# Kernel optimization log

Hardware: AMD Instinct MI355X
Metric: run time of the kernel (lower is better)

The kernel has to match this reference:

```python
import jax, jax.numpy as jnp
import numpy as np

IN_F = 512
OUT_F = 512
ALPHA = 0.2  # LeakyReLU negative slope
# dropout p=0.1 is a no-op at inference (training=False), so omitted


def setup_inputs() -> dict:
    key = jax.random.key(0)
    k1, k2, k3 = jax.random.split(key, 3)
    B, N = 16, 1024
    x = jax.random.normal(k1, (B, N, IN_F), dtype=jnp.float32)
    # xavier_uniform with gain=1.414
    limW = 1.414 * np.sqrt(6.0 / (IN_F + OUT_F))
    W = jax.random.uniform(k2, (IN_F, OUT_F), minval=-limW, maxval=limW, dtype=jnp.float32)
    lima = 1.414 * np.sqrt(6.0 / (2 * OUT_F + 1))
    a = jax.random.uniform(k3, (2 * OUT_F, 1), minval=-lima, maxval=lima, dtype=jnp.float32)
    beta = jnp.ones((1,), dtype=jnp.float32)
    return {"x": x, "W": W, "a": a, "beta": beta}


def reference(x, W, a, beta):
    # h: [B, N, F]
    h = jnp.matmul(x, W)
    # Split attention vector: e_ij = leakyrelu(h_i . a1 + h_j . a2)
    a1 = a[:OUT_F, 0]   # [F]
    a2 = a[OUT_F:, 0]   # [F]
    s1 = jnp.einsum('bnf,f->bn', h, a1)  # [B, N]
    s2 = jnp.einsum('bnf,f->bn', h, a2)  # [B, N]
    e = s1[:, :, None] + s2[:, None, :]  # [B, N, N]
    e = jnp.where(e > 0, e, ALPHA * e)   # LeakyReLU
    attention = jax.nn.softmax(e, axis=2)
    h_prime = jnp.einsum('bnm,bmf->bnf', attention, h)
    out = jax.nn.elu(h_prime + beta * h)
    return out
```

## Files before the change

### kernel.cpp

```cpp
#include <hip/hip_runtime.h>

using u16 = unsigned short;
using u32 = unsigned int;
using u64 = unsigned long long;

#define ALPHA 0.2f
#define LOG2E 1.4426950408889634f

typedef __bf16 bf16x8 __attribute__((ext_vector_type(8)));
typedef float f32x4 __attribute__((ext_vector_type(4)));
typedef float f32x16 __attribute__((ext_vector_type(16)));

__device__ __forceinline__ u16 f2bf(float f) {
  u32 u = __builtin_bit_cast(u32, f);
  u += 0x7FFFu + ((u >> 16) & 1u);
  return (u16)(u >> 16);
}
__device__ __forceinline__ float bf2f(u16 h) {
  u32 u = ((u32)h) << 16;
  return __builtin_bit_cast(float, u);
}
__device__ __forceinline__ void gload_lds16(const void* g, void* l) {
  __builtin_amdgcn_global_load_lds((__attribute__((address_space(1))) void*)g,
                                   (__attribute__((address_space(3))) void*)l,
                                   16, 0, 0);
}

__global__ __launch_bounds__(256) void k_cast_wT(const float* __restrict__ W, u16* __restrict__ wbt) {
  int idx = blockIdx.x * 256 + threadIdx.x;
  int k = idx >> 9, n = idx & 511;
  wbt[n * 512 + k] = f2bf(W[idx]);
}

__global__ __launch_bounds__(256, 2) void k_gemm1(const float* __restrict__ x, const u16* __restrict__ wbt,
                                                  const float* __restrict__ a,
                                                  u16* __restrict__ hbf,
                                                  float* __restrict__ s1p, float* __restrict__ s2p) {
  __shared__ __attribute__((aligned(16))) char lds[73728];
  __shared__ __attribute__((aligned(16))) float a_l[256];

  const int t = threadIdx.x;
  const int lane = t & 63;
  const int w = t >> 6;
  const int l31 = lane & 31, lhi = lane >> 5;
  const int rb = w >> 1, cg = w & 1;
  const int g = blockIdx.x;
  const int cb = (g >> 3) & 3;
  const int tile_m = (g & 7) | ((g >> 5) << 3);
  const int row0 = tile_m * 128;
  const int col0 = cb * 128;

  a_l[t] = (t < 128) ? a[col0 + t] : a[512 + col0 + (t - 128)];

  f32x16 acc[2][2];
#pragma unroll
  for (int i = 0; i < 2; ++i)
#pragma unroll
    for (int j = 0; j < 2; ++j)
#pragma unroll
      for (int r = 0; r < 16; ++r) acc[i][j][r] = 0.f;

#define STAGE_G1(kt, Ab, Bb)                                                              \
  {                                                                                       \
    const int k0_ = (kt) * 32;                                                            \
    _Pragma("unroll")                                                                     \
    for (int i = 0; i < 4; ++i) {                                                         \
      int G = i * 256 + t;                                                                \
      int row = G >> 3, ks = G & 7;                                                       \
      gload_lds16(x + (size_t)(row0 + row) * 512 + k0_ + ((ks ^ (row & 7)) * 4),          \
                  (Ab) + (size_t)(i * 256 + w * 64) * 16);                                \
    }                                                                                     \
    _Pragma("unroll")                                                                     \
    for (int i = 0; i < 2; ++i) {                                                         \
      int G = i * 256 + t;                                                                \
      int col = G >> 2, ks = G & 3;                                                       \
      gload_lds16(wbt + (size_t)(col0 + col) * 512 + k0_ + ((ks ^ ((col >> 1) & 3)) * 8), \
                  (Bb) + (size_t)(i * 256 + w * 64) * 16);                                \
    }                                                                                     \
  }

#define COMPUTE_G1(Ab, Bb)                                                                         \
  {                                                                                                \
    _Pragma("unroll")                                                                              \
    for (int ks = 0; ks < 2; ++ks) {                                                               \
      bf16x8 af[2];                                                                                \
      _Pragma("unroll")                                                                            \
      for (int sub = 0; sub < 2; ++sub) {                                                          \
        const int arow = rb * 64 + sub * 32 + l31;                                                 \
        const int kg = ks * 4 + lhi * 2;                                                           \
        f32x4 fa0 = *reinterpret_cast<const f32x4*>((Ab) + (size_t)(arow * 8 + (kg ^ (arow & 7))) * 16); \
        f32x4 fa1 = *reinterpret_cast<const f32x4*>((Ab) + (size_t)(arow * 8 + ((kg + 1) ^ (arow & 7))) * 16); \
        _Pragma("unroll")                                                                          \
        for (int jj = 0; jj < 4; ++jj) {                                                           \
          af[sub][jj] = (__bf16)fa0[jj];                                                           \
          af[sub][jj + 4] = (__bf16)fa1[jj];                                                       \
        }                                                                                          \
      }                                                                                            \
      bf16x8 bfr[2];                                                                               \
      _Pragma("unroll")                                                                            \
      for (int bt = 0; bt < 2; ++bt) {                                                             \
        const int bcol = cg * 64 + bt * 32 + l31;                                                  \
        const int kslot = (ks * 2 + lhi) ^ ((bcol >> 1) & 3);                                      \
        bfr[bt] = *reinterpret_cast<const bf16x8*>((Bb) + (size_t)(bcol * 4 + kslot) * 16);        \
      }                                                                                            \
      _Pragma("unroll")                                                                            \
      for (int sub = 0; sub < 2; ++sub)                                                            \
        _Pragma("unroll")                                                                          \
        for (int bt = 0; bt < 2; ++bt)                                                             \
          acc[sub][bt] = __builtin_amdgcn_mfma_f32_32x32x16_bf16(af[sub], bfr[bt], acc[sub][bt], 0, 0, 0); \
    }                                                                                              \
  }

  char* Ac = lds;             char* Bc = lds + 49152;
  char* An = lds + 16384;     char* Bn = lds + 57344;
  char* As = lds + 32768;     char* Bs = lds + 65536;

  STAGE_G1(0, Ac, Bc);
  STAGE_G1(1, An, Bn);
  __builtin_amdgcn_sched_barrier(0);
  asm volatile("s_waitcnt vmcnt(6) lgkmcnt(0)" ::: "memory");
  __builtin_amdgcn_s_barrier();
  __builtin_amdgcn_sched_barrier(0);

#pragma unroll 1
  for (int kt = 0; kt < 14; ++kt) {
    STAGE_G1(kt + 2, As, Bs);
    COMPUTE_G1(Ac, Bc);
    __builtin_amdgcn_sched_barrier(0);
    asm volatile("s_waitcnt vmcnt(6)" ::: "memory");
    __builtin_amdgcn_s_barrier();
    __builtin_amdgcn_sched_barrier(0);
    char* ta = Ac; Ac = An; An = As; As = ta;
    char* tb = Bc; Bc = Bn; Bn = Bs; Bs = tb;
  }
  COMPUTE_G1(Ac, Bc);
  __builtin_amdgcn_sched_barrier(0);
  asm volatile("s_waitcnt vmcnt(0)" ::: "memory");
  __builtin_amdgcn_s_barrier();
  __builtin_amdgcn_sched_barrier(0);
  COMPUTE_G1(An, Bn);
#undef STAGE_G1
#undef COMPUTE_G1

  __syncthreads();

  u16* lT = (u16*)lds;
#pragma unroll
  for (int sub = 0; sub < 2; ++sub)
#pragma unroll
    for (int bt = 0; bt < 2; ++bt) {
      const int col = cg * 64 + bt * 32 + l31;
#pragma unroll
      for (int r = 0; r < 16; ++r) {
        int row = rb * 64 + sub * 32 + (r & 3) + 8 * (r >> 2) + 4 * lhi;
        lT[row * 136 + col] = f2bf(acc[sub][bt][r]);
      }
    }
  __syncthreads();

#pragma unroll
  for (int i = 0; i < 8; ++i) {
    int G = i * 256 + t;
    int row = G >> 4, gg = G & 15;
    uint4 v = *reinterpret_cast<const uint4*>(&lT[row * 136 + gg * 8]);
    *reinterpret_cast<uint4*>(&hbf[(size_t)(row0 + row) * 512 + col0 + gg * 8]) = v;
  }
  {
    const int r2 = t >> 1, half = t & 1;
    float d1 = 0.f, d2 = 0.f;
#pragma unroll
    for (int i = 0; i < 8; ++i) {
      uint4 v = *reinterpret_cast<const uint4*>(&lT[r2 * 136 + half * 64 + i * 8]);
      u32 wds[4] = {v.x, v.y, v.z, v.w};
#pragma unroll
      for (int jj = 0; jj < 8; ++jj) {
        float h = bf2f((u16)(wds[jj >> 1] >> ((jj & 1) * 16)));
        d1 += h * a_l[half * 64 + i * 8 + jj];
        d2 += h * a_l[128 + half * 64 + i * 8 + jj];
      }
    }
    d1 += __shfl_xor(d1, 1);
    d2 += __shfl_xor(d2, 1);
    if (half == 0) {
      s1p[cb * 16384 + row0 + r2] = d1;
      s2p[cb * 16384 + row0 + r2] = d2;
    }
  }
}

__global__ __launch_bounds__(1024) void k_prep(const float* __restrict__ s1p, const float* __restrict__ s2p,
                                               float* __restrict__ e1s, float* __restrict__ e2s,
                                               u32* __restrict__ permM, u32* __restrict__ kng,
                                               float* __restrict__ c1ig, float* __restrict__ c2ig) {
  __shared__ u32 sk[1024];
  __shared__ float s2all[1024];
  __shared__ float s2sv[1024];
  __shared__ float arrA[1024];
  __shared__ float arrB[1024];
  const int b = blockIdx.x;
  const int t = threadIdx.x;
  const int id = b * 1024 + t;

  const float s1v = (s1p[id] + s1p[16384 + id] + s1p[32768 + id] + s1p[49152 + id]) * LOG2E;
  const float s2v = (s2p[id] + s2p[16384 + id] + s2p[32768 + id] + s2p[49152 + id]) * LOG2E;
  s2all[t] = s2v;

  {
    u32 bits = __builtin_bit_cast(u32, s2v);
    u32 key = (bits & 0x80000000u) ? ~bits : (bits | 0x80000000u);
    sk[t] = (key & 0xFFFFFC00u) | (u32)t;
  }
  for (int size = 2; size <= 1024; size <<= 1)
    for (int stride = size >> 1; stride > 0; stride >>= 1) {
      __syncthreads();
      int ixj = t ^ stride;
      if (ixj > t) {
        u32 va = sk[t], vb = sk[ixj];
        bool asc = ((t & size) == 0);
        if ((va > vb) == asc) { sk[t] = vb; sk[ixj] = va; }
      }
    }
  __syncthreads();

  const u32 idx = sk[t] & 1023u;
  const float sv = s2all[idx];
  s2sv[t] = sv;
  __syncthreads();

  const float E1 = exp2f(sv), E2 = exp2f(ALPHA * sv);
  e1s[b * 1024 + t] = E1;
  e2s[b * 1024 + t] = E2;
  permM[b * 1024 + t] = idx;
  arrA[t] = E2;
  arrB[t] = exp2f(s2sv[1023 - t]);
  __syncthreads();

  for (int off = 1; off < 1024; off <<= 1) {
    float aA = (t >= off) ? arrA[t - off] : 0.f;
    float aB = (t >= off) ? arrB[t - off] : 0.f;
    __syncthreads();
    arrA[t] += aA;
    arrB[t] += aB;
    __syncthreads();
  }

  {
    const float thr = -s1v;
    int lo = 0, hi = 1024;
    while (lo < hi) { int mid = (lo + hi) >> 1; if (s2sv[mid] <= thr) lo = mid + 1; else hi = mid; }
    const int kn = lo;
    float se1suf = (kn == 1024) ? 0.f : arrB[1023 - kn];
    float se2pre = (kn == 0) ? 0.f : arrA[kn - 1];
    const float c1 = exp2f(s1v), c2 = exp2f(ALPHA * s1v);
    const float inv = 1.0f / (c1 * se1suf + c2 * se2pre);
    c1ig[id] = c1 * inv;
    c2ig[id] = c2 * inv;
    kng[id] = (u32)kn;
  }
}

__global__ __launch_bounds__(256, 2) void k_sweep2(const u16* __restrict__ hbf,
                                                   const float* __restrict__ e1s, const float* __restrict__ e2s,
                                                   const u32* __restrict__ permM, const u32* __restrict__ kng,
                                                   const float* __restrict__ c1ig, const float* __restrict__ c2ig,
                                                   const float* __restrict__ betag, float* __restrict__ out) {
  __shared__ u16 Cp1[1025][16];
  __shared__ u16 Cp2[1025][16];
  __shared__ float c1i_l[1024];
  __shared__ float c2i_l[1024];
  __shared__ u16 kn_l[1024];
  __shared__ float segS1[16][16];
  __shared__ float segP2[16][16];

  const int t = threadIdx.x;
  const int B = blockIdx.x;
  const int b = (B & 7) * 2 + ((B >> 3) & 1);
  const int fc = B >> 4;

  const u16* hB = hbf + (size_t)b * 1024 * 512 + fc * 16;

#pragma unroll
  for (int q = 0; q < 4; ++q) {
    int i = q * 256 + t;
    c1i_l[i] = c1ig[b * 1024 + i];
    c2i_l[i] = c2ig[b * 1024 + i];
    kn_l[i] = (u16)kng[b * 1024 + i];
  }

  const int f = t & 15;
  const int seg = t >> 4;
  const int i0 = seg * 64;
  const u32* permB = permM + b * 1024 + i0;
  const float* e1B = e1s + b * 1024 + i0;
  const float* e2B = e2s + b * 1024 + i0;

  u32 hpk[32];
  float ss1 = 0.f, ss2 = 0.f;
#pragma unroll 8
  for (int c = 0; c < 64; c += 2) {
    u16 h0 = hB[(size_t)permB[c] * 512 + f];
    u16 h1 = hB[(size_t)permB[c + 1] * 512 + f];
    hpk[c >> 1] = (u32)h0 | ((u32)h1 << 16);
    ss1 = fmaf(e1B[c], bf2f(h0), ss1);
    ss1 = fmaf(e1B[c + 1], bf2f(h1), ss1);
    ss2 = fmaf(e2B[c], bf2f(h0), ss2);
    ss2 = fmaf(e2B[c + 1], bf2f(h1), ss2);
  }
  segS1[seg][f] = ss1;
  segP2[seg][f] = ss2;
  __syncthreads();

  float sufAfter = 0.f, preBefore = 0.f;
#pragma unroll
  for (int s7 = 0; s7 < 16; ++s7) {
    if (s7 > seg) sufAfter += segS1[s7][f];
    if (s7 < seg) preBefore += segP2[s7][f];
  }

  if (seg == 15) Cp1[1024][f] = 0;
  {
    float run1 = sufAfter;
#pragma unroll
    for (int c = 63; c >= 0; --c) {
      u16 hv = (u16)((hpk[c >> 1] >> ((c & 1) * 16)) & 0xFFFFu);
      run1 = fmaf(e1B[c], bf2f(hv), run1);
      Cp1[i0 + c][f] = f2bf(run1);
    }
  }
  {
    float run2 = preBefore;
#pragma unroll
    for (int c = 0; c < 64; ++c) {
      Cp2[i0 + c][f] = f2bf(run2);
      u16 hv = (u16)((hpk[c >> 1] >> ((c & 1) * 16)) & 0xFFFFu);
      run2 = fmaf(e2B[c], bf2f(hv), run2);
    }
    if (seg == 15) Cp2[1024][f] = f2bf(run2);
  }
  __syncthreads();

  const float beta = betag[0];
  const int nl = t >> 4;
#pragma unroll 4
  for (int r = 0; r < 64; ++r) {
    const int n = r * 16 + nl;
    const int kn = kn_l[n];
    const float A = bf2f(Cp1[kn][f]);
    const float Bv = bf2f(Cp2[kn][f]);
    const float hvn = bf2f(hB[(size_t)n * 512 + f]);
    const float xv = c1i_l[n] * A + c2i_l[n] * Bv + beta * hvn;
    out[((size_t)b * 1024 + n) * 512 + fc * 16 + f] = xv > 0.f ? xv : __expf(xv) - 1.0f;
  }
}

extern "C" void kernel_launch(void* const* d_in, const int* in_sizes, int n_in,
                              void* d_out, int out_size, void* d_ws, size_t ws_size,
                              hipStream_t stream) {
  const float* x = (const float*)d_in[0];
  const float* W = (const float*)d_in[1];
  const float* a = (const float*)d_in[2];
  const float* beta = (const float*)d_in[3];
  float* out = (float*)d_out;

  char* ws = (char*)d_ws;
  u16* hbf = (u16*)ws;
  char* sm = ws + (16u << 20);
  float* e1s = (float*)(sm);
  float* e2s = (float*)(sm + (64u << 10));
  u32* permM = (u32*)(sm + (128u << 10));
  u32* kng = (u32*)(sm + (192u << 10));
  float* c1i = (float*)(sm + (256u << 10));
  float* c2i = (float*)(sm + (320u << 10));
  float* s1p = (float*)(sm + (512u << 10));
  float* s2p = (float*)(sm + (768u << 10));
  u16* wbt = (u16*)(sm + (1024u << 10));

  k_cast_wT<<<1024, 256, 0, stream>>>(W, wbt);
  k_gemm1<<<512, 256, 0, stream>>>(x, wbt, a, hbf, s1p, s2p);
  k_prep<<<16, 1024, 0, stream>>>(s1p, s2p, e1s, e2s, permM, kng, c1i, c2i);
  k_sweep2<<<512, 256, 0, stream>>>(hbf, e1s, e2s, permM, kng, c1i, c2i, beta, out);
}
```

Before: 66.64 us.

## Double sweep block size, interleave prefix arrays in padded LDS, read coefficients from global

The sweep kernel now runs 512 threads per block, so each thread scans a 32-row segment instead of 64. This shortens the serial prefix/suffix chains and halves per-thread register arrays. The two bf16 prefix arrays are packed into one padded u32 LDS array, so the final pass needs a single LDS read per row. The per-row coefficient and split-index staging in LDS is removed in favour of direct global loads. The trade-off is extra global traffic for those coefficients in the output loop, plus a longer cross-segment reduction over 32 segments.

```diff
diff --git a/kernel.cpp b/kernel.cpp
--- a/kernel.cpp
+++ b/kernel.cpp
@@ -259,18 +259,14 @@
   }
 }
 
-__global__ __launch_bounds__(256, 2) void k_sweep2(const u16* __restrict__ hbf,
+__global__ __launch_bounds__(512, 2) void k_sweep2(const u16* __restrict__ hbf,
                                                    const float* __restrict__ e1s, const float* __restrict__ e2s,
                                                    const u32* __restrict__ permM, const u32* __restrict__ kng,
                                                    const float* __restrict__ c1ig, const float* __restrict__ c2ig,
                                                    const float* __restrict__ betag, float* __restrict__ out) {
-  __shared__ u16 Cp1[1025][16];
-  __shared__ u16 Cp2[1025][16];
-  __shared__ float c1i_l[1024];
-  __shared__ float c2i_l[1024];
-  __shared__ u16 kn_l[1024];
-  __shared__ float segS1[16][16];
-  __shared__ float segP2[16][16];
+  __shared__ u32 Cp[1025][17];
+  __shared__ float segS1[32][16];
+  __shared__ float segP2[32][16];
 
   const int t = threadIdx.x;
   const int B = blockIdx.x;
@@ -279,25 +275,17 @@
 
   const u16* hB = hbf + (size_t)b * 1024 * 512 + fc * 16;
 
-#pragma unroll
-  for (int q = 0; q < 4; ++q) {
-    int i = q * 256 + t;
-    c1i_l[i] = c1ig[b * 1024 + i];
-    c2i_l[i] = c2ig[b * 1024 + i];
-    kn_l[i] = (u16)kng[b * 1024 + i];
-  }
-
   const int f = t & 15;
   const int seg = t >> 4;
-  const int i0 = seg * 64;
+  const int i0 = seg * 32;
   const u32* permB = permM + b * 1024 + i0;
   const float* e1B = e1s + b * 1024 + i0;
   const float* e2B = e2s + b * 1024 + i0;
 
-  u32 hpk[32];
+  u32 hpk[16];
   float ss1 = 0.f, ss2 = 0.f;
-#pragma unroll 8
-  for (int c = 0; c < 64; c += 2) {
+#pragma unroll
+  for (int c = 0; c < 32; c += 2) {
     u16 h0 = hB[(size_t)permB[c] * 512 + f];
     u16 h1 = hB[(size_t)permB[c + 1] * 512 + f];
     hpk[c >> 1] = (u32)h0 | ((u32)h1 << 16);
@@ -312,43 +300,49 @@
 
   float sufAfter = 0.f, preBefore = 0.f;
 #pragma unroll
-  for (int s7 = 0; s7 < 16; ++s7) {
+  for (int s7 = 0; s7 < 32; ++s7) {
     if (s7 > seg) sufAfter += segS1[s7][f];
     if (s7 < seg) preBefore += segP2[s7][f];
   }
 
-  if (seg == 15) Cp1[1024][f] = 0;
+  u32 c1p[16];
   {
     float run1 = sufAfter;
 #pragma unroll
-    for (int c = 63; c >= 0; --c) {
-      u16 hv = (u16)((hpk[c >> 1] >> ((c & 1) * 16)) & 0xFFFFu);
+    for (int c = 31; c >= 0; --c) {
+      u16 hv = (u16)(hpk[c >> 1] >> ((c & 1) * 16));
       run1 = fmaf(e1B[c], bf2f(hv), run1);
-      Cp1[i0 + c][f] = f2bf(run1);
+      if (c & 1) c1p[c >> 1] = (u32)f2bf(run1) << 16;
+      else c1p[c >> 1] |= (u32)f2bf(run1);
     }
   }
   {
     float run2 = preBefore;
 #pragma unroll
-    for (int c = 0; c < 64; ++c) {
-      Cp2[i0 + c][f] = f2bf(run2);
-      u16 hv = (u16)((hpk[c >> 1] >> ((c & 1) * 16)) & 0xFFFFu);
+    for (int c = 0; c < 32; ++c) {
+      u16 c1v = (u16)(c1p[c >> 1] >> ((c & 1) * 16));
+      Cp[i0 + c][f] = (u32)c1v | ((u32)f2bf(run2) << 16);
+      u16 hv = (u16)(hpk[c >> 1] >> ((c & 1) * 16));
       run2 = fmaf(e2B[c], bf2f(hv), run2);
     }
-    if (seg == 15) Cp2[1024][f] = f2bf(run2);
+    if (seg == 31) Cp[1024][f] = (u32)f2bf(run2) << 16;
   }
   __syncthreads();
 
   const float beta = betag[0];
   const int nl = t >> 4;
+  const u32* knB = kng + b * 1024;
+  const float* c1B = c1ig + b * 1024;
+  const float* c2B = c2ig + b * 1024;
 #pragma unroll 4
-  for (int r = 0; r < 64; ++r) {
-    const int n = r * 16 + nl;
-    const int kn = kn_l[n];
-    const float A = bf2f(Cp1[kn][f]);
-    const float Bv = bf2f(Cp2[kn][f]);
+  for (int r = 0; r < 32; ++r) {
+    const int n = r * 32 + nl;
+    const int kn = (int)knB[n];
+    const u32 cp = Cp[kn][f];
+    const float A = bf2f((u16)(cp & 0xFFFFu));
+    const float Bv = bf2f((u16)(cp >> 16));
     const float hvn = bf2f(hB[(size_t)n * 512 + f]);
-    const float xv = c1i_l[n] * A + c2i_l[n] * Bv + beta * hvn;
+    const float xv = c1B[n] * A + c2B[n] * Bv + beta * hvn;
     out[((size_t)b * 1024 + n) * 512 + fc * 16 + f] = xv > 0.f ? xv : __expf(xv) - 1.0f;
   }
 }
@@ -378,5 +372,5 @@
   k_cast_wT<<<1024, 256, 0, stream>>>(W, wbt);
   k_gemm1<<<512, 256, 0, stream>>>(x, wbt, a, hbf, s1p, s2p);
   k_prep<<<16, 1024, 0, stream>>>(s1p, s2p, e1s, e2s, permM, kng, c1i, c2i);
-  k_sweep2<<<512, 256, 0, stream>>>(hbf, e1s, e2s, permM, kng, c1i, c2i, beta, out);
-}
+  k_sweep2<<<512, 512, 0, stream>>>(hbf, e1s, e2s, permM, kng, c1i, c2i, beta, out);
+}
```

Measured after the change: 72.57 us. +8.9%, slower.

## Use wave shuffles in prep sort/scan and interleave padded prefix tables

Applied to the files above, without the earlier changes.

In k_prep, the bitonic sort now does its intra-wavefront stages (stride below 64) with __shfl_xor compare-exchange instead of shared memory and barriers. The prefix scans now use a wave-level shfl_up scan plus a cross-wave offset pass, which replaces the 10-step barrier-heavy Hillis-Steele scan. In k_sweep2, the two bf16 prefix tables are merged into one u32 array padded by one row per 64-row segment, so the gather does one LDS read per element and bank conflicts drop. The intent is to cut barrier count and LDS traffic, at the cost of more register pressure from the packed c1p array.

```diff
diff --git a/kernel.cpp b/kernel.cpp
--- a/kernel.cpp
+++ b/kernel.cpp
@@ -197,21 +197,42 @@
   __shared__ float s2sv[1024];
   __shared__ float arrA[1024];
   __shared__ float arrB[1024];
+  __shared__ float wtA[16], wtB[16];
   const int b = blockIdx.x;
   const int t = threadIdx.x;
+  const int lane = t & 63, wid = t >> 6;
   const int id = b * 1024 + t;
 
   const float s1v = (s1p[id] + s1p[16384 + id] + s1p[32768 + id] + s1p[49152 + id]) * LOG2E;
   const float s2v = (s2p[id] + s2p[16384 + id] + s2p[32768 + id] + s2p[49152 + id]) * LOG2E;
   s2all[t] = s2v;
 
+  u32 key;
   {
     u32 bits = __builtin_bit_cast(u32, s2v);
-    u32 key = (bits & 0x80000000u) ? ~bits : (bits | 0x80000000u);
-    sk[t] = (key & 0xFFFFFC00u) | (u32)t;
-  }
-  for (int size = 2; size <= 1024; size <<= 1)
-    for (int stride = size >> 1; stride > 0; stride >>= 1) {
+    u32 k2 = (bits & 0x80000000u) ? ~bits : (bits | 0x80000000u);
+    key = (k2 & 0xFFFFFC00u) | (u32)t;
+  }
+
+#define SHFL_CE(size_, stride_)                                            \
+  {                                                                        \
+    u32 partner = (u32)__shfl_xor((int)key, (stride_));                    \
+    bool dir = ((t & (size_)) == 0);                                       \
+    bool keepMin = (dir == ((t & (stride_)) == 0));                        \
+    key = keepMin ? (key < partner ? key : partner)                        \
+                  : (key > partner ? key : partner);                       \
+  }
+
+#pragma unroll
+  for (int size = 2; size <= 64; size <<= 1)
+#pragma unroll
+    for (int stride = size >> 1; stride > 0; stride >>= 1) SHFL_CE(size, stride);
+
+#pragma unroll 1
+  for (int size = 128; size <= 1024; size <<= 1) {
+    sk[t] = key;
+#pragma unroll 1
+    for (int stride = size >> 1; stride >= 64; stride >>= 1) {
       __syncthreads();
       int ixj = t ^ stride;
       if (ixj > t) {
@@ -220,9 +241,14 @@
         if ((va > vb) == asc) { sk[t] = vb; sk[ixj] = va; }
       }
     }
-  __syncthreads();
-
-  const u32 idx = sk[t] & 1023u;
+    __syncthreads();
+    key = sk[t];
+#pragma unroll
+    for (int stride = 32; stride > 0; stride >>= 1) SHFL_CE(size, stride);
+  }
+#undef SHFL_CE
+
+  const u32 idx = key & 1023u;
   const float sv = s2all[idx];
   s2sv[t] = sv;
   __syncthreads();
@@ -231,18 +257,30 @@
   e1s[b * 1024 + t] = E1;
   e2s[b * 1024 + t] = E2;
   permM[b * 1024 + t] = idx;
-  arrA[t] = E2;
-  arrB[t] = exp2f(s2sv[1023 - t]);
-  __syncthreads();
-
-  for (int off = 1; off < 1024; off <<= 1) {
-    float aA = (t >= off) ? arrA[t - off] : 0.f;
-    float aB = (t >= off) ? arrB[t - off] : 0.f;
-    __syncthreads();
-    arrA[t] += aA;
-    arrB[t] += aB;
-    __syncthreads();
-  }
+
+  float aA = E2;
+  float aB = exp2f(s2sv[1023 - t]);
+#pragma unroll
+  for (int off = 1; off < 64; off <<= 1) {
+    float uA = __shfl_up(aA, off);
+    float uB = __shfl_up(aB, off);
+    if (lane >= off) { aA += uA; aB += uB; }
+  }
+  if (lane == 63) { wtA[wid] = aA; wtB[wid] = aB; }
+  __syncthreads();
+  {
+    float offA = 0.f, offB = 0.f;
+#pragma unroll
+    for (int i2 = 0; i2 < 16; ++i2) {
+      float vA2 = wtA[i2], vB2 = wtB[i2];
+      if (i2 < wid) { offA += vA2; offB += vB2; }
+    }
+    aA += offA;
+    aB += offB;
+  }
+  arrA[t] = aA;
+  arrB[t] = aB;
+  __syncthreads();
 
   {
     const float thr = -s1v;
@@ -264,8 +302,7 @@
                                                    const u32* __restrict__ permM, const u32* __restrict__ kng,
                                                    const float* __restrict__ c1ig, const float* __restrict__ c2ig,
                                                    const float* __restrict__ betag, float* __restrict__ out) {
-  __shared__ u16 Cp1[1025][16];
-  __shared__ u16 Cp2[1025][16];
+  __shared__ u32 Cp[1041][16];
   __shared__ float c1i_l[1024];
   __shared__ float c2i_l[1024];
   __shared__ u16 kn_l[1024];
@@ -290,6 +327,7 @@
   const int f = t & 15;
   const int seg = t >> 4;
   const int i0 = seg * 64;
+  const int p0 = i0 + seg;
   const u32* permB = permM + b * 1024 + i0;
   const float* e1B = e1s + b * 1024 + i0;
   const float* e2B = e2s + b * 1024 + i0;
@@ -317,25 +355,27 @@
     if (s7 < seg) preBefore += segP2[s7][f];
   }
 
-  if (seg == 15) Cp1[1024][f] = 0;
+  u32 c1p[32];
   {
     float run1 = sufAfter;
 #pragma unroll
     for (int c = 63; c >= 0; --c) {
-      u16 hv = (u16)((hpk[c >> 1] >> ((c & 1) * 16)) & 0xFFFFu);
+      u16 hv = (u16)(hpk[c >> 1] >> ((c & 1) * 16));
       run1 = fmaf(e1B[c], bf2f(hv), run1);
-      Cp1[i0 + c][f] = f2bf(run1);
+      if (c & 1) c1p[c >> 1] = (u32)f2bf(run1) << 16;
+      else c1p[c >> 1] |= (u32)f2bf(run1);
     }
   }
   {
     float run2 = preBefore;
 #pragma unroll
     for (int c = 0; c < 64; ++c) {
-      Cp2[i0 + c][f] = f2bf(run2);
-      u16 hv = (u16)((hpk[c >> 1] >> ((c & 1) * 16)) & 0xFFFFu);
+      u16 c1v = (u16)(c1p[c >> 1] >> ((c & 1) * 16));
+      Cp[p0 + c][f] = (u32)c1v | ((u32)f2bf(run2) << 16);
+      u16 hv = (u16)(hpk[c >> 1] >> ((c & 1) * 16));
       run2 = fmaf(e2B[c], bf2f(hv), run2);
     }
-    if (seg == 15) Cp2[1024][f] = f2bf(run2);
+    if (seg == 15) Cp[1040][f] = (u32)f2bf(run2) << 16;
   }
   __syncthreads();
 
@@ -345,8 +385,9 @@
   for (int r = 0; r < 64; ++r) {
     const int n = r * 16 + nl;
     const int kn = kn_l[n];
-    const float A = bf2f(Cp1[kn][f]);
-    const float Bv = bf2f(Cp2[kn][f]);
+    const u32 cp = Cp[kn + (kn >> 6)][f];
+    const float A = bf2f((u16)(cp & 0xFFFFu));
+    const float Bv = bf2f((u16)(cp >> 16));
     const float hvn = bf2f(hB[(size_t)n * 512 + f]);
     const float xv = c1i_l[n] * A + c2i_l[n] * Bv + beta * hvn;
     out[((size_t)b * 1024 + n) * 512 + fc * 16 + f] = xv > 0.f ? xv : __expf(xv) - 1.0f;
```

After: 62.13 us. 6.8% less time.
